# Performance work log

Hardware: AMD Instinct MI355X
Metric: run time of the kernel (lower is better)

The kernel has to match this reference:

```python
import jax, jax.numpy as jnp
import numpy as np
import math

B, S, HID, H = 4, 4096, 1024, 16
DH = HID // H  # 64

def setup_inputs() -> dict:
    key = jax.random.key(0)
    ks = jax.random.split(key, 6)
    query = jax.random.normal(ks[0], (B, S, HID), dtype=jnp.float32)
    key_t = jax.random.normal(ks[1], (B, S, HID), dtype=jnp.float32)
    value = jax.random.normal(ks[2], (B, S, HID), dtype=jnp.float32)
    attn_mask = jax.random.normal(ks[3], (B, S, H, H), dtype=jnp.float32)
    # nn.Linear(hidden, 3*hidden): weight (3H, H), bias (3H,)
    W_qkv = jax.random.normal(ks[4], (3 * HID, HID), dtype=jnp.float32) * (1.0 / math.sqrt(HID))
    b_qkv = jax.random.normal(ks[5], (3 * HID,), dtype=jnp.float32) * 0.01
    return {"query": query, "key": key_t, "value": value, "attn_mask": attn_mask,
            "W_qkv": W_qkv, "b_qkv": b_qkv}

def reference(query, key, value, attn_mask, W_qkv, b_qkv):
    # fused QKV projection (only `query` is used, matching the source)
    qkv = jnp.einsum('bsh,oh->bso', query, W_qkv) + b_qkv  # (B,S,3*HID)
    q, k, v = jnp.split(qkv, 3, axis=-1)
    q = q.reshape(B, S, H, DH)
    k = k.reshape(B, S, H, DH)
    v = v.reshape(B, S, H, DH)
    # NOTE: no (B,H,S,D) permute in the source -> scores are head-vs-head per position
    scale = 1.0 / math.sqrt(DH)
    qk = jnp.einsum('bshd,bsgd->bshg', q, k) * scale + attn_mask  # (B,S,H,H)
    attn_weight = jax.nn.softmax(qk, axis=-1)
    # dropout_p=0 (eval): identity
    o = jnp.einsum('bshg,bsgd->bshd', attn_weight, v)  # (B,S,H,DH)
    return o.reshape(B, S, HID)
```

## Files before the change

kernel.cpp:

```cpp
#include <hip/hip_runtime.h>
#include <cstdint>
#include <cstddef>


typedef __attribute__((ext_vector_type(8))) short bf16x8;
typedef __attribute__((ext_vector_type(4))) float f32x4;

__device__ inline unsigned short f2bf(float f) {
  unsigned int i = __float_as_uint(f);
  i += 0x7fff + ((i >> 16) & 1);
  return (unsigned short)(i >> 16);
}

__device__ inline void async16(const void* g, void* l) {
  __builtin_amdgcn_global_load_lds(
      (const __attribute__((address_space(1))) void*)g,
      (__attribute__((address_space(3))) void*)l, 16, 0, 0);
}

__device__ inline void unpack8(bf16x8 v, float* f) {
  union { bf16x8 s; unsigned int u[4]; } x; x.s = v;
  #pragma unroll
  for (int i = 0; i < 4; ++i) {
    f[2 * i]     = __uint_as_float(x.u[i] << 16);
    f[2 * i + 1] = __uint_as_float(x.u[i] & 0xffff0000u);
  }
}

__global__ __launch_bounds__(256) void cast_kernel(const float* __restrict__ in,
                                                   unsigned short* __restrict__ out,
                                                   int n) {
  int i = (blockIdx.x * 256 + threadIdx.x) * 4;
  if (i >= n) return;
  float4 v = *(const float4*)(in + i);
  union { unsigned short u[4]; unsigned long long ll; } o;
  o.u[0] = f2bf(v.x); o.u[1] = f2bf(v.y); o.u[2] = f2bf(v.z); o.u[3] = f2bf(v.w);
  *(unsigned long long*)(out + i) = o.ll;
}

#define GK 1024
#define GN 3072
__global__ __launch_bounds__(512, 2) void gemm_qkv(const unsigned short* __restrict__ A,
                                                   const unsigned short* __restrict__ Bm,
                                                   const float* __restrict__ bias,
                                                   unsigned short* __restrict__ C) {
  __shared__ unsigned short As[2][256][64];
  __shared__ unsigned short Bs[2][256][64];

  const int bid = blockIdx.x;
  const int swz = (bid & 7) * 96 + (bid >> 3);
  const int m0 = (swz / 12) * 256;
  const int n0 = (swz % 12) * 256;

  const int tid  = threadIdx.x;
  const int lane = tid & 63;
  const int wave = tid >> 6;
  const int wm = wave & 1;
  const int wn = wave >> 1;
  const int fr = lane & 15;
  const int fq = lane >> 4;

  const int r0 = tid >> 3;
  const int c0 = (tid & 7) ^ (r0 & 7);
  const unsigned short* gA = A  + (size_t)(m0 + r0) * GK + c0 * 8;
  const unsigned short* gB = Bm + (size_t)(n0 + r0) * GK + c0 * 8;
  const int ls0 = wave * 512;

#define STAGE_A(tt, hh) do {                                                   \
    unsigned short* lb_ = &As[(tt) & 1][(hh) * 128][0];                        \
    const unsigned short* g_ = gA + (size_t)(hh) * 128 * GK + (tt) * 64;       \
    async16(g_, lb_ + ls0);                                                    \
    async16(g_ + (size_t)64 * GK, lb_ + 4096 + ls0);                           \
  } while (0)
#define STAGE_B(tt, hh) do {                                                   \
    unsigned short* lb_ = &Bs[(tt) & 1][(hh) * 128][0];                        \
    const unsigned short* g_ = gB + (size_t)(hh) * 128 * GK + (tt) * 64;       \
    async16(g_, lb_ + ls0);                                                    \
    async16(g_ + (size_t)64 * GK, lb_ + 4096 + ls0);                           \
  } while (0)

  f32x4 acc[8][4] = {};

  STAGE_A(0, 0); STAGE_A(0, 1); STAGE_B(0, 0); STAGE_B(0, 1);
  STAGE_B(1, 0); STAGE_A(1, 0); STAGE_B(1, 1);

  for (int t = 0; t < 16; ++t) {
    const int cur = t & 1;
    if (t < 15) { asm volatile("s_waitcnt vmcnt(6)" ::: "memory"); }
    else        { asm volatile("s_waitcnt vmcnt(0)" ::: "memory"); }
    __builtin_amdgcn_s_barrier();
    __builtin_amdgcn_sched_barrier(0);

    bf16x8 bfr[4][2];
    #pragma unroll
    for (int p = 0; p < 4; ++p) {
      bf16x8 af[2][2];
      #pragma unroll
      for (int ii = 0; ii < 2; ++ii) {
        const int rA = (p * 2 + ii) * 32 + wm * 16 + fr;
        #pragma unroll
        for (int ks = 0; ks < 2; ++ks)
          af[ii][ks] = *(const bf16x8*)&As[cur][rA][((ks * 4 + fq) ^ (rA & 7)) * 8];
      }
      if (p == 0) {
        #pragma unroll
        for (int j = 0; j < 4; ++j) {
          const int rB = wn * 64 + j * 16 + fr;
          #pragma unroll
          for (int ks = 0; ks < 2; ++ks)
            bfr[j][ks] = *(const bf16x8*)&Bs[cur][rB][((ks * 4 + fq) ^ (rB & 7)) * 8];
        }
      }
      if (p == 1 && t + 1 < 16) { STAGE_A(t + 1, 1); }
      if (p == 2 && t + 2 < 16) { STAGE_B(t + 2, 0); }
      if (p == 3 && t + 2 < 16) { STAGE_A(t + 2, 0); STAGE_B(t + 2, 1); }

      __builtin_amdgcn_s_barrier();
      __builtin_amdgcn_sched_barrier(0);
      __builtin_amdgcn_s_setprio(1);
      #pragma unroll
      for (int ks = 0; ks < 2; ++ks)
        #pragma unroll
        for (int ii = 0; ii < 2; ++ii)
          #pragma unroll
          for (int j = 0; j < 4; ++j)
            acc[p * 2 + ii][j] = __builtin_amdgcn_mfma_f32_16x16x32_bf16(
                af[ii][ks], bfr[j][ks], acc[p * 2 + ii][j], 0, 0, 0);
      __builtin_amdgcn_s_setprio(0);
      __builtin_amdgcn_sched_barrier(0);
    }
  }
#undef STAGE_A
#undef STAGE_B

  #pragma unroll
  for (int j = 0; j < 4; ++j) {
    const int col = n0 + wn * 64 + j * 16 + fr;
    const float bc = bias[col];
    #pragma unroll
    for (int i = 0; i < 8; ++i) {
      const int rowb = m0 + i * 32 + wm * 16 + fq * 4;
      #pragma unroll
      for (int rr = 0; rr < 4; ++rr)
        C[(size_t)(rowb + rr) * GN + col] = f2bf(acc[i][j][rr] + bc);
    }
  }
}

__global__ __launch_bounds__(256) void attn_kernel(const unsigned short* __restrict__ QKV,
                                                   const float* __restrict__ mask,
                                                   float* __restrict__ out) {
  __shared__ unsigned short shKV[4][2048];
  const int wave = threadIdx.x >> 6;
  const int lane = threadIdx.x & 63;
  const int pos = blockIdx.x * 4 + wave;

  const unsigned short* row = QKV + (size_t)pos * 3072;

  #pragma unroll
  for (int t = 0; t < 4; ++t)
    async16(&row[1024 + t * 512 + (size_t)lane * 8], &shKV[wave][t * 512]);

  bf16x8 q0 = *(const bf16x8*)&row[lane * 16];
  bf16x8 q1 = *(const bf16x8*)&row[lane * 16 + 8];

  const int h = lane >> 2;
  const int dg = lane & 3;

  const float* mrow = mask + (size_t)pos * 256 + h * 16;
  float4 m4[4];
  #pragma unroll
  for (int t = 0; t < 4; ++t) m4[t] = *(const float4*)&mrow[t * 4];

  float q[16];
  unpack8(q0, q);
  unpack8(q1, q + 8);

  asm volatile("s_waitcnt vmcnt(0)" ::: "memory");

  float s[16];
  #pragma unroll
  for (int g = 0; g < 16; ++g) {
    const unsigned short* kp = &shKV[wave][g * 64 + dg * 16];
    float kf[16];
    unpack8(*(const bf16x8*)kp, kf);
    unpack8(*(const bf16x8*)(kp + 8), kf + 8);
    float acc = 0.f;
    #pragma unroll
    for (int d = 0; d < 16; ++d) acc += q[d] * kf[d];
    s[g] = acc;
  }
  #pragma unroll
  for (int g = 0; g < 16; ++g) {
    s[g] += __shfl_xor(s[g], 1);
    s[g] += __shfl_xor(s[g], 2);
  }

  const float* mp = (const float*)m4;
  float mx = -1e30f;
  #pragma unroll
  for (int g = 0; g < 16; ++g) {
    s[g] = s[g] * 0.125f + mp[g];
    mx = fmaxf(mx, s[g]);
  }
  float sum = 0.f;
  #pragma unroll
  for (int g = 0; g < 16; ++g) { s[g] = __expf(s[g] - mx); sum += s[g]; }
  float inv = 1.f / sum;

  float o[16];
  #pragma unroll
  for (int dd = 0; dd < 16; ++dd) o[dd] = 0.f;
  #pragma unroll
  for (int g = 0; g < 16; ++g) {
    const unsigned short* vp = &shKV[wave][1024 + g * 64 + dg * 16];
    float vf[16];
    unpack8(*(const bf16x8*)vp, vf);
    unpack8(*(const bf16x8*)(vp + 8), vf + 8);
    float p = s[g];
    #pragma unroll
    for (int dd = 0; dd < 16; ++dd) o[dd] += p * vf[dd];
  }

  float* op = out + (size_t)pos * 1024 + lane * 16;
  #pragma unroll
  for (int t = 0; t < 4; ++t) {
    float4 w;
    w.x = o[t * 4 + 0] * inv; w.y = o[t * 4 + 1] * inv;
    w.z = o[t * 4 + 2] * inv; w.w = o[t * 4 + 3] * inv;
    *(float4*)(op + t * 4) = w;
  }
}

extern "C" void kernel_launch(void* const* d_in, const int* in_sizes, int n_in,
                              void* d_out, int out_size, void* d_ws, size_t ws_size,
                              hipStream_t stream) {
  const float* query = (const float*)d_in[0];
  const float* mask  = (const float*)d_in[3];
  const float* Wqkv  = (const float*)d_in[4];
  const float* bqkv  = (const float*)d_in[5];
  float* out = (float*)d_out;

  unsigned short* qb   = (unsigned short*)d_ws;
  unsigned short* wb   = (unsigned short*)((char*)d_ws + 33554432);
  unsigned short* qkvb = (unsigned short*)((char*)d_ws + 39845888);

  cast_kernel<<<16384, 256, 0, stream>>>(query, qb, 16777216);
  cast_kernel<<<3072, 256, 0, stream>>>(Wqkv, wb, 3145728);

  gemm_qkv<<<768, 512, 0, stream>>>(qb, wb, bqkv, qkvb);

  attn_kernel<<<4096, 256, 0, stream>>>(qkvb, mask, out);
}
```

Before: 356.2 us.

## Software-pipeline LDS fragment reads ahead of MFMA phases in QKV GEMM

Restructures the QKV GEMM main loop so each MFMA phase runs on fragments that were already loaded from LDS. The reads for the next phase, and for the next tile's first phase, are issued right after the current phase's MFMAs. Global-to-LDS staging is rescheduled so the two tiles in flight are fully prefetched, with a single vmcnt(0) wait in the middle of each iteration. The aim is to hide LDS read latency behind matrix-core work and cut the stalls between phases. The cost is more live fragment registers and a barrier schedule that is more delicate to keep correct.

```diff
diff --git a/kernel.cpp b/kernel.cpp
--- a/kernel.cpp
+++ b/kernel.cpp
@@ -79,66 +79,81 @@
     async16(g_ + (size_t)64 * GK, lb_ + 4096 + ls0);                           \
   } while (0)
 
+#define READ_A4(bp, ph) do {                                                   \
+    _Pragma("unroll")                                                          \
+    for (int ii = 0; ii < 2; ++ii) {                                           \
+      const int rA = ((ph) * 2 + ii) * 32 + wm * 16 + fr;                      \
+      _Pragma("unroll")                                                        \
+      for (int ks = 0; ks < 2; ++ks)                                           \
+        af[ii][ks] = *(const bf16x8*)&As[bp][rA][((ks * 4 + fq) ^ (rA & 7)) * 8]; \
+    } } while (0)
+
+#define READ_B8(bp) do {                                                       \
+    _Pragma("unroll")                                                          \
+    for (int j = 0; j < 4; ++j) {                                              \
+      const int rB = wn * 64 + j * 16 + fr;                                    \
+      _Pragma("unroll")                                                        \
+      for (int ks = 0; ks < 2; ++ks)                                           \
+        bfr[j][ks] = *(const bf16x8*)&Bs[bp][rB][((ks * 4 + fq) ^ (rB & 7)) * 8]; \
+    } } while (0)
+
+#define MFMA_PHASE(ph) do {                                                    \
+    __builtin_amdgcn_s_setprio(1);                                             \
+    _Pragma("unroll")                                                          \
+    for (int ks = 0; ks < 2; ++ks)                                             \
+      _Pragma("unroll")                                                        \
+      for (int ii = 0; ii < 2; ++ii)                                           \
+        _Pragma("unroll")                                                      \
+        for (int j = 0; j < 4; ++j)                                            \
+          acc[(ph) * 2 + ii][j] = __builtin_amdgcn_mfma_f32_16x16x32_bf16(     \
+              af[ii][ks], bfr[j][ks], acc[(ph) * 2 + ii][j], 0, 0, 0);         \
+    __builtin_amdgcn_s_setprio(0);                                             \
+  } while (0)
+
   f32x4 acc[8][4] = {};
+  bf16x8 af[2][2];
+  bf16x8 bfr[4][2];
 
   STAGE_A(0, 0); STAGE_A(0, 1); STAGE_B(0, 0); STAGE_B(0, 1);
-  STAGE_B(1, 0); STAGE_A(1, 0); STAGE_B(1, 1);
+  STAGE_A(1, 0); STAGE_A(1, 1); STAGE_B(1, 0); STAGE_B(1, 1);
+  asm volatile("s_waitcnt vmcnt(8)\n\ts_barrier" ::: "memory");
+  __builtin_amdgcn_sched_barrier(0);
+  READ_A4(0, 0);
+  READ_B8(0);
 
   for (int t = 0; t < 16; ++t) {
-    const int cur = t & 1;
-    if (t < 15) { asm volatile("s_waitcnt vmcnt(6)" ::: "memory"); }
-    else        { asm volatile("s_waitcnt vmcnt(0)" ::: "memory"); }
-    __builtin_amdgcn_s_barrier();
-    __builtin_amdgcn_sched_barrier(0);
-
-    bf16x8 bfr[4][2];
-    #pragma unroll
-    for (int p = 0; p < 4; ++p) {
-      bf16x8 af[2][2];
-      #pragma unroll
-      for (int ii = 0; ii < 2; ++ii) {
-        const int rA = (p * 2 + ii) * 32 + wm * 16 + fr;
-        #pragma unroll
-        for (int ks = 0; ks < 2; ++ks)
-          af[ii][ks] = *(const bf16x8*)&As[cur][rA][((ks * 4 + fq) ^ (rA & 7)) * 8];
-      }
-      if (p == 0) {
-        #pragma unroll
-        for (int j = 0; j < 4; ++j) {
-          const int rB = wn * 64 + j * 16 + fr;
-          #pragma unroll
-          for (int ks = 0; ks < 2; ++ks)
-            bfr[j][ks] = *(const bf16x8*)&Bs[cur][rB][((ks * 4 + fq) ^ (rB & 7)) * 8];
-        }
-      }
-      if (p == 1 && t + 1 < 16) { STAGE_A(t + 1, 1); }
-      if (p == 2 && t + 2 < 16) { STAGE_B(t + 2, 0); }
-      if (p == 3 && t + 2 < 16) { STAGE_A(t + 2, 0); STAGE_B(t + 2, 1); }
-
-      __builtin_amdgcn_s_barrier();
-      __builtin_amdgcn_sched_barrier(0);
-      __builtin_amdgcn_s_setprio(1);
-      #pragma unroll
-      for (int ks = 0; ks < 2; ++ks)
-        #pragma unroll
-        for (int ii = 0; ii < 2; ++ii)
-          #pragma unroll
-          for (int j = 0; j < 4; ++j)
-            acc[p * 2 + ii][j] = __builtin_amdgcn_mfma_f32_16x16x32_bf16(
-                af[ii][ks], bfr[j][ks], acc[p * 2 + ii][j], 0, 0, 0);
-      __builtin_amdgcn_s_setprio(0);
-      __builtin_amdgcn_sched_barrier(0);
-    }
+    const int cur = t & 1, nxt = cur ^ 1;
+    asm volatile("s_waitcnt lgkmcnt(0)\n\ts_barrier" ::: "memory");
+    __builtin_amdgcn_sched_barrier(0);
+    MFMA_PHASE(0);
+    READ_A4(cur, 1);
+    asm volatile("s_waitcnt lgkmcnt(0)\n\ts_barrier" ::: "memory");
+    __builtin_amdgcn_sched_barrier(0);
+    MFMA_PHASE(1);
+    READ_A4(cur, 2);
+    asm volatile("s_waitcnt vmcnt(0) lgkmcnt(0)\n\ts_barrier" ::: "memory");
+    __builtin_amdgcn_sched_barrier(0);
+    MFMA_PHASE(2);
+    READ_A4(cur, 3);
+    if (t + 2 < 16) { STAGE_B(t + 2, 0); }
+    asm volatile("s_waitcnt lgkmcnt(0)\n\ts_barrier" ::: "memory");
+    __builtin_amdgcn_sched_barrier(0);
+    MFMA_PHASE(3);
+    if (t + 1 < 16) { READ_A4(nxt, 0); READ_B8(nxt); }
+    if (t + 2 < 16) { STAGE_A(t + 2, 0); STAGE_A(t + 2, 1); STAGE_B(t + 2, 1); }
   }
 #undef STAGE_A
 #undef STAGE_B
-
-  #pragma unroll
-  for (int j = 0; j < 4; ++j) {
-    const int col = n0 + wn * 64 + j * 16 + fr;
-    const float bc = bias[col];
+#undef READ_A4
+#undef READ_B8
+#undef MFMA_PHASE
+
+  #pragma unroll
+  for (int i = 0; i < 8; ++i) {
     #pragma unroll
-    for (int i = 0; i < 8; ++i) {
+    for (int j = 0; j < 4; ++j) {
+      const int col = n0 + wn * 64 + j * 16 + fr;
+      const float bc = bias[col];
       const int rowb = m0 + i * 32 + wm * 16 + fq * 4;
       #pragma unroll
       for (int rr = 0; rr < 4; ++rr)
```

New measurement: 340.5 us. 1.05x faster.
